# Optimization experiments

Hardware: AMD Instinct MI355X
Metric: run time of the kernel (lower is better)

Reference implementation:

```python
import jax, jax.numpy as jnp
import numpy as np

N_NODES = 50000
N_EDGES = 800000
N_FEAT = 128
N_HID = 256
N_PAIRS = 100000


def _gcn_norm(edge_index, n_nodes):
    # add self loops, compute D^-1/2 (A+I) D^-1/2 edge weights (PyG gcn_norm)
    loops = jnp.arange(n_nodes, dtype=edge_index.dtype)
    row = jnp.concatenate([edge_index[0], loops])
    col = jnp.concatenate([edge_index[1], loops])
    deg = jax.ops.segment_sum(jnp.ones_like(col, dtype=jnp.float32), col,
                              num_segments=n_nodes)
    dinv = jnp.where(deg > 0, jax.lax.rsqrt(deg), 0.0)
    norm = dinv[row] * dinv[col]  # [E + N]
    return row, col, norm


def _gcn_conv(x, W, b, row, col, norm, n_nodes):
    h = x @ W                       # [N, out]
    msg = h[row] * norm[:, None]    # gather + scale  [E+N, out]
    agg = jax.ops.segment_sum(msg, col, num_segments=n_nodes)  # scatter-add
    return agg + b


def setup_inputs() -> dict:
    key = jax.random.key(0)
    ks = jax.random.split(key, 9)
    edge_index = jax.random.randint(ks[0], (2, N_EDGES), 0, N_NODES, dtype=jnp.int64)
    features = jax.random.normal(ks[1], (N_NODES, N_FEAT), dtype=jnp.float32)
    mask = jax.random.randint(ks[2], (N_PAIRS, 2), 0, N_NODES, dtype=jnp.int64)
    s1 = 1.0 / np.sqrt(N_FEAT)
    s2 = 1.0 / np.sqrt(N_HID)
    W1 = jax.random.uniform(ks[3], (N_FEAT, N_HID), jnp.float32, -s1, s1)
    b1 = jnp.zeros((N_HID,), jnp.float32)
    W2 = jax.random.uniform(ks[4], (N_HID, N_FEAT), jnp.float32, -s2, s2)
    b2 = jnp.zeros((N_FEAT,), jnp.float32)
    Wl = jax.random.uniform(ks[5], (N_HID, 1), jnp.float32, -s2, s2)
    bl = jax.random.uniform(ks[6], (1,), jnp.float32, -s2, s2)
    return {"edge_index": edge_index, "features": features, "mask": mask,
            "W1": W1, "b1": b1, "W2": W2, "b2": b2, "Wl": Wl, "bl": bl}


def reference(edge_index, features, mask, W1, b1, W2, b2, Wl, bl):
    n = features.shape[0]
    row, col, norm = _gcn_norm(edge_index, n)
    h = _gcn_conv(features, W1, b1, row, col, norm, n)   # GCNConv a
    h = jax.nn.relu(h)                                   # dropout p=0 -> identity
    h = _gcn_conv(h, W2, b2, row, col, norm, n)          # GCNConv b
    mt = mask.T
    p1 = jax.lax.stop_gradient(h[mt[0]])                 # .detach()
    p2 = jax.lax.stop_gradient(h[mt[1]])
    hp = jnp.concatenate([p1, p2], axis=1)               # [n_pairs, 2*n_feat]
    return jax.nn.sigmoid(hp @ Wl + bl)
```

## Files before the change

### kernel.cpp

```cpp
#include <hip/hip_runtime.h>
#include <math.h>

#define NFEAT 128
#define NHID 256
#define NBLK 128

typedef __attribute__((ext_vector_type(8))) short short8;
typedef __attribute__((ext_vector_type(4))) float f32x4;
typedef __attribute__((ext_vector_type(2))) float f32x2;

__device__ inline unsigned short f2bf(float f) {
  unsigned u = __float_as_uint(f);
  u += 0x7fffu + ((u >> 16) & 1u);
  return (unsigned short)(u >> 16);
}
__device__ inline float bflo(unsigned u) { return __uint_as_float(u << 16); }
__device__ inline float bfhi(unsigned u) { return __uint_as_float(u & 0xffff0000u); }


__device__ inline void packOne(const float* __restrict__ W,
                               unsigned short* __restrict__ Wp, int idx, int KS,
                               int OUT) {
  int lane = idx & 63;
  int t = idx >> 6;
  int ks = t % KS;
  int nt = t / KS;
  int n = nt * 16 + (lane & 15);
  int k0 = ks * 32 + (lane >> 4) * 8;
  unsigned short v[8];
#pragma unroll
  for (int j = 0; j < 8; j++) v[j] = f2bf(W[(size_t)(k0 + j) * OUT + n]);
  *reinterpret_cast<short8*>(Wp + (size_t)idx * 8) =
      *reinterpret_cast<short8*>(v);
}

__global__ __launch_bounds__(1024) void k_hist_pack(
    const int* __restrict__ col, int* __restrict__ hist2d, int nE, int nb,
    const float* __restrict__ W1, const float* __restrict__ W2,
    unsigned short* __restrict__ W1p, unsigned short* __restrict__ W2p) {
  if (blockIdx.x >= NBLK) {
    int idx = (blockIdx.x - NBLK) * 1024 + threadIdx.x;
    if (idx < 4096) packOne(W1, W1p, idx, 4, 256);
    else packOne(W2, W2p, idx - 4096, 8, 128);
    return;
  }
  __shared__ int h[1024];
  for (int i = threadIdx.x; i < nb; i += 1024) h[i] = 0;
  __syncthreads();
  int chunk = (nE + NBLK - 1) / NBLK;
  int beg = blockIdx.x * chunk, end = min(beg + chunk, nE);
  for (int e = beg + threadIdx.x; e < end; e += 1024)
    atomicAdd(&h[col[e] >> 6], 1);
  __syncthreads();
  for (int i = threadIdx.x; i < nb; i += 1024)
    hist2d[i * NBLK + blockIdx.x] = h[i];
}

__global__ __launch_bounds__(256) void k_bsum(const int* __restrict__ a,
                                              int* __restrict__ psum, int S,
                                              const float* __restrict__ b2,
                                              const float* __restrict__ Wl,
                                              const float* __restrict__ bl,
                                              float* __restrict__ Cbuf) {
  int t = threadIdx.x;
  if (blockIdx.x == gridDim.x - 1) {
    float v = (t < 128) ? b2[t] * (Wl[t] + Wl[128 + t]) : 0.f;
#pragma unroll
    for (int o = 32; o; o >>= 1) v += __shfl_down(v, o);
    __shared__ float fw[4];
    if ((t & 63) == 0) fw[t >> 6] = v;
    __syncthreads();
    if (t == 0) Cbuf[0] = fw[0] + fw[1] + fw[2] + fw[3] + bl[0];
    return;
  }
  int i = blockIdx.x * 256 + t;
  int v = (i < S) ? a[i] : 0;
#pragma unroll
  for (int o = 32; o; o >>= 1) v += __shfl_down(v, o);
  __shared__ int ws[4];
  if ((t & 63) == 0) ws[t >> 6] = v;
  __syncthreads();
  if (t == 0) psum[blockIdx.x] = ws[0] + ws[1] + ws[2] + ws[3];
}

__global__ __launch_bounds__(256) void k_s3m(const int* __restrict__ a,
                                             const int* __restrict__ psum,
                                             int* __restrict__ out, int S) {
  __shared__ int sh[256];
  __shared__ int ws[4];
  int t = threadIdx.x;
  int b = blockIdx.x;
  int partial = 0;
  for (int i = t; i < b; i += 256) partial += psum[i];
#pragma unroll
  for (int o = 32; o; o >>= 1) partial += __shfl_down(partial, o);
  if ((t & 63) == 0) ws[t >> 6] = partial;
  int i = b * 256 + t;
  int d = (i < S) ? a[i] : 0;
  sh[t] = d;
  __syncthreads();
  int base = ws[0] + ws[1] + ws[2] + ws[3];
  for (int o = 1; o < 256; o <<= 1) {
    int u = (t >= o) ? sh[t - o] : 0;
    __syncthreads();
    sh[t] += u;
    __syncthreads();
  }
  if (i < S) out[i] = base + sh[t] - d;
}

__global__ __launch_bounds__(1024) void k_part2(const int* __restrict__ row,
                                                const int* __restrict__ col,
                                                const int* __restrict__ sbase,
                                                unsigned* __restrict__ tmp,
                                                int nE, int nb) {
  __shared__ int cur[1024];
  for (int i = threadIdx.x; i < nb; i += 1024)
    cur[i] = sbase[i * NBLK + blockIdx.x];
  __syncthreads();
  int chunk = (nE + NBLK - 1) / NBLK;
  int beg = blockIdx.x * chunk, end = min(beg + chunk, nE);
  for (int e = beg + threadIdx.x; e < end; e += 1024) {
    int c = col[e];
    int pos = atomicAdd(&cur[c >> 6], 1);
    tmp[pos] = ((unsigned)(c & 63) << 16) | (unsigned)row[e];
  }
}

__global__ __launch_bounds__(256) void k_bsort_cvt(
    const unsigned* __restrict__ tmp, const int* __restrict__ sbase,
    int* __restrict__ ebuf, int* __restrict__ offs, float* __restrict__ dinv,
    const float* __restrict__ feat, unsigned short* __restrict__ xs, int n,
    int nE, int nb) {
  __shared__ int bins[64], cur[64];
  __shared__ float sdinv[64];
  int b = blockIdx.x;
  int beg = sbase[b * NBLK];
  int end = (b == nb - 1) ? nE : sbase[(b + 1) * NBLK];
  int t = threadIdx.x;
  if (t == 0 && b == nb - 1) offs[n] = nE;
  if (t < 64) bins[t] = 0;
  __syncthreads();
  for (int i = beg + t; i < end; i += 256) atomicAdd(&bins[tmp[i] >> 16], 1);
  __syncthreads();
  if (t < 64) {
    int v = bins[t];
    int s = v;
#pragma unroll
    for (int o = 1; o < 64; o <<= 1) {
      int u = __shfl_up(s, o);
      if (t >= o) s += u;
    }
    int off = beg + s - v;
    cur[t] = off;
    float dv = rsqrtf((float)(v + 1));
    sdinv[t] = dv;
    int node = b * 64 + t;
    if (node < n) {
      offs[node] = off;
      dinv[node] = dv;
    }
  }
  __syncthreads();
  for (int i = beg + t; i < end; i += 256) {
    unsigned p = tmp[i];
    int pos = atomicAdd(&cur[p >> 16], 1);
    ebuf[pos] = (int)(p & 0xffffu);
  }
  for (int i = t; i < 64 * 32; i += 256) {
    int r = i >> 5;
    int node = b * 64 + r;
    if (node >= n) break;
    float d = sdinv[r];
    float4 v = reinterpret_cast<const float4*>(feat)[(size_t)node * 32 + (i & 31)];
    unsigned short o[4] = {f2bf(v.x * d), f2bf(v.y * d), f2bf(v.z * d),
                           f2bf(v.w * d)};
    reinterpret_cast<ushort4*>(xs)[(size_t)node * 32 + (i & 31)] =
        *reinterpret_cast<ushort4*>(o);
  }
}

__global__ __launch_bounds__(256) void k_fused(
    const char* __restrict__ Gb, const int* __restrict__ offs,
    const int* __restrict__ ebuf, const float* __restrict__ dinv,
    const unsigned short* __restrict__ B1p, const unsigned short* __restrict__ B2p,
    const float* __restrict__ b1, const float* __restrict__ Wl,
    float* __restrict__ P, int n) {
  __shared__ __align__(16) unsigned short sh_z[32 * 128];
  __shared__ __align__(16) unsigned short sh1[32 * 264];
  __shared__ float pacc[32][2];
  int rt0 = blockIdx.x * 2;
  int wave = threadIdx.x >> 6;
  int lane = threadIdx.x & 63;
  int quad = lane >> 4;
  if (threadIdx.x < 64) pacc[threadIdx.x >> 1][threadIdx.x & 1] = 0.f;

  {
    int g = lane >> 4;
    int c = lane & 15;
    unsigned cb = (unsigned)c << 4;
    int rbase = rt0 * 16;
    for (int it = 0; it < 8; ++it) {
      int rin = wave * 8 + it;
      int node = rbase + rin;
      f32x2 acc[4] = {};
      float d = 0.f;
      if (node < n) {
        d = dinv[node];
        int beg = offs[node], end = offs[node + 1];
        if (g == 0) {
          uint4 s = *reinterpret_cast<const uint4*>(
              Gb + (((unsigned)node << 8) | cb));
          acc[0] = (f32x2){bflo(s.x), bfhi(s.x)};
          acc[1] = (f32x2){bflo(s.y), bfhi(s.y)};
          acc[2] = (f32x2){bflo(s.z), bfhi(s.z)};
          acc[3] = (f32x2){bflo(s.w), bfhi(s.w)};
        }
        int e = beg + g;
        for (; e + 4 < end; e += 8) {
          int i0 = ebuf[e], i1 = ebuf[e + 4];
          uint4 v0 = *reinterpret_cast<const uint4*>(
              Gb + (((unsigned)i0 << 8) | cb));
          uint4 v1 = *reinterpret_cast<const uint4*>(
              Gb + (((unsigned)i1 << 8) | cb));
          acc[0] += (f32x2){bflo(v0.x), bfhi(v0.x)};
          acc[1] += (f32x2){bflo(v0.y), bfhi(v0.y)};
          acc[2] += (f32x2){bflo(v0.z), bfhi(v0.z)};
          acc[3] += (f32x2){bflo(v0.w), bfhi(v0.w)};
          acc[0] += (f32x2){bflo(v1.x), bfhi(v1.x)};
          acc[1] += (f32x2){bflo(v1.y), bfhi(v1.y)};
          acc[2] += (f32x2){bflo(v1.z), bfhi(v1.z)};
          acc[3] += (f32x2){bflo(v1.w), bfhi(v1.w)};
        }
        if (e < end) {
          uint4 v0 = *reinterpret_cast<const uint4*>(
              Gb + (((unsigned)ebuf[e] << 8) | cb));
          acc[0] += (f32x2){bflo(v0.x), bfhi(v0.x)};
          acc[1] += (f32x2){bflo(v0.y), bfhi(v0.y)};
          acc[2] += (f32x2){bflo(v0.z), bfhi(v0.z)};
          acc[3] += (f32x2){bflo(v0.w), bfhi(v0.w)};
        }
      }
#pragma unroll
      for (int j = 0; j < 4; j++) {
        acc[j].x += __shfl_down(acc[j].x, 32);
        acc[j].y += __shfl_down(acc[j].y, 32);
        acc[j].x += __shfl_down(acc[j].x, 16);
        acc[j].y += __shfl_down(acc[j].y, 16);
      }
      if (g == 0) {
        unsigned o[4];
#pragma unroll
        for (int k = 0; k < 4; k++)
          o[k] = (unsigned)f2bf(acc[k].x * d) |
                 ((unsigned)f2bf(acc[k].y * d) << 16);
        int c_swz = c ^ (rin & 7);
        *reinterpret_cast<uint4*>(sh_z + rin * 128 + c_swz * 8) =
            *reinterpret_cast<uint4*>(o);
      }
    }
  }
  __syncthreads();

  f32x4 acc[2][4] = {};
  int r0a = lane & 15;
  int xsw = lane & 7;
#pragma unroll
  for (int ks = 0; ks < 4; ks++) {
    int cA = quad + ks * 4;
    int cS = (cA ^ xsw) * 8;
    short8 a0 = *reinterpret_cast<const short8*>(sh_z + r0a * 128 + cS);
    short8 a1 = *reinterpret_cast<const short8*>(sh_z + (16 + r0a) * 128 + cS);
#pragma unroll
    for (int ct = 0; ct < 4; ct++) {
      int nt = wave * 4 + ct;
      short8 b = *reinterpret_cast<const short8*>(
          B1p + ((size_t)(nt * 4 + ks) * 64 + lane) * 8);
      acc[0][ct] = __builtin_amdgcn_mfma_f32_16x16x32_bf16(a0, b, acc[0][ct], 0, 0, 0);
      acc[1][ct] = __builtin_amdgcn_mfma_f32_16x16x32_bf16(a1, b, acc[1][ct], 0, 0, 0);
    }
  }
#pragma unroll
  for (int ct = 0; ct < 4; ct++) {
    int c = (wave * 4 + ct) * 16 + (lane & 15);
    float bv = b1[c];
#pragma unroll
    for (int rg = 0; rg < 2; rg++)
#pragma unroll
      for (int i = 0; i < 4; i++) {
        float v = fmaxf(acc[rg][ct][i] + bv, 0.f);
        sh1[(rg * 16 + quad * 4 + i) * 264 + c] = f2bf(v);
      }
  }
  __syncthreads();

  f32x4 acc2[2][2] = {};
  const unsigned short* a2_0 = sh1 + (size_t)(lane & 15) * 264 + quad * 8;
  const unsigned short* a2_1 = sh1 + (size_t)(16 + (lane & 15)) * 264 + quad * 8;
#pragma unroll
  for (int ks = 0; ks < 8; ks++) {
    short8 a0 = *reinterpret_cast<const short8*>(a2_0 + ks * 32);
    short8 a1 = *reinterpret_cast<const short8*>(a2_1 + ks * 32);
#pragma unroll
    for (int ct = 0; ct < 2; ct++) {
      int nt = wave * 2 + ct;
      short8 b = *reinterpret_cast<const short8*>(
          B2p + ((size_t)(nt * 8 + ks) * 64 + lane) * 8);
      acc2[0][ct] = __builtin_amdgcn_mfma_f32_16x16x32_bf16(a0, b, acc2[0][ct], 0, 0, 0);
      acc2[1][ct] = __builtin_amdgcn_mfma_f32_16x16x32_bf16(a1, b, acc2[1][ct], 0, 0, 0);
    }
  }
  float p1[2][4] = {}, p2[2][4] = {};
#pragma unroll
  for (int rg = 0; rg < 2; rg++) {
    int r0 = (rt0 + rg) * 16 + quad * 4;
    float dv[4];
#pragma unroll
    for (int i = 0; i < 4; i++) dv[i] = dinv[r0 + i];
#pragma unroll
    for (int ct = 0; ct < 2; ct++) {
      int c = (wave * 2 + ct) * 16 + (lane & 15);
      float wl1 = Wl[c], wl2 = Wl[128 + c];
#pragma unroll
      for (int i = 0; i < 4; i++) {
        float v = acc2[rg][ct][i] * dv[i];
        p1[rg][i] = fmaf(v, wl1, p1[rg][i]);
        p2[rg][i] = fmaf(v, wl2, p2[rg][i]);
      }
    }
  }
#pragma unroll
  for (int rg = 0; rg < 2; rg++)
#pragma unroll
    for (int i = 0; i < 4; i++) {
#pragma unroll
      for (int o = 8; o; o >>= 1) {
        p1[rg][i] += __shfl_xor(p1[rg][i], o);
        p2[rg][i] += __shfl_xor(p2[rg][i], o);
      }
    }
  if ((lane & 15) == 0) {
#pragma unroll
    for (int rg = 0; rg < 2; rg++)
#pragma unroll
      for (int i = 0; i < 4; i++) {
        int row = rg * 16 + quad * 4 + i;
        atomicAdd(&pacc[row][0], p1[rg][i]);
        atomicAdd(&pacc[row][1], p2[rg][i]);
      }
  }
  __syncthreads();
// ... 19 lines not shown
    sy += v.y;
  }
  sx += __shfl_down(sx, 2);
  sy += __shfl_down(sy, 2);
  sx += __shfl_down(sx, 1);
  sy += __shfl_down(sy, 1);
  if (sub == 0) {
    float2 self = p[i];
    float d = dinv[i];
    q[i] = make_float2((sx + self.x) * d, (sy + self.y) * d);
  }
}

__global__ __launch_bounds__(256) void k_head2(const float2* __restrict__ q,
                                               const int* __restrict__ mask,
                                               const float* __restrict__ Cbuf,
                                               float* __restrict__ out, int P) {
  int p = blockIdx.x * 256 + threadIdx.x;
  if (p >= P) return;
  int m0 = mask[2 * p], m1 = mask[2 * p + 1];
  float s = q[m0].x + q[m1].y + Cbuf[0];
  out[p] = 1.0f / (1.0f + expf(-s));
}

extern "C" void kernel_launch(void* const* d_in, const int* in_sizes, int n_in,
                              void* d_out, int out_size, void* d_ws,
                              size_t ws_size, hipStream_t stream) {
  const int* edge = (const int*)d_in[0];
  const float* feat = (const float*)d_in[1];
  const int* mask = (const int*)d_in[2];
  const float* W1 = (const float*)d_in[3];
  const float* b1 = (const float*)d_in[4];
  const float* W2 = (const float*)d_in[5];
  const float* b2 = (const float*)d_in[6];
  const float* Wl = (const float*)d_in[7];
  const float* bl = (const float*)d_in[8];
  float* out = (float*)d_out;

  const int E = in_sizes[0] / 2;
  const int N = in_sizes[1] / NFEAT;
  const int P = in_sizes[2] / 2;
  const int* rowp = edge;
  const int* colp = edge + E;
  const int nrt = N / 16;
  const int nb = (N + 63) / 64;
  const int S = nb * NBLK;
  const int nS = (S + 255) / 256;

  auto aln = [](size_t x) { return (x + 255) & ~(size_t)255; };
  char* w = (char*)d_ws;
  int* hist2d = (int*)w;           w += aln((size_t)S * 4);
  int* sbase = (int*)w;            w += aln((size_t)S * 4);
  int* psum = (int*)w;             w += aln((size_t)1024 * 4);
  float* Cbuf = (float*)w;         w += aln(256);
  int* offs = (int*)w;             w += aln((size_t)(N + 1) * 4);
  int* ebuf = (int*)w;             w += aln((size_t)E * 4);
  unsigned* tmp = (unsigned*)w;    w += aln((size_t)E * 4);
  float* dinv = (float*)w;         w += aln((size_t)N * 4 + 1024);
  unsigned short* xs = (unsigned short*)w;  w += aln((size_t)N * NFEAT * 2);
  float* p = (float*)w;            w += aln((size_t)(N + 32) * 8);
  float2* q = (float2*)w;          w += aln((size_t)N * 8);
  unsigned short* W1p = (unsigned short*)w; w += aln((size_t)NFEAT * NHID * 2);
  unsigned short* W2p = (unsigned short*)w; w += aln((size_t)NHID * NFEAT * 2);

  k_hist_pack<<<NBLK + 8, 1024, 0, stream>>>(colp, hist2d, E, nb, W1, W2, W1p,
                                             W2p);
  k_bsum<<<nS + 1, 256, 0, stream>>>(hist2d, psum, S, b2, Wl, bl, Cbuf);
  k_s3m<<<nS, 256, 0, stream>>>(hist2d, psum, sbase, S);
  k_part2<<<NBLK, 1024, 0, stream>>>(rowp, colp, sbase, tmp, E, nb);
  k_bsort_cvt<<<nb, 256, 0, stream>>>(tmp, sbase, ebuf, offs, dinv, feat, xs,
                                      N, E, nb);
  k_fused<<<(nrt + 1) / 2, 256, 0, stream>>>((const char*)xs, offs, ebuf, dinv,
                                             W1p, W2p, b1, Wl, p, N);
  k_agg_s<<<(N + 63) / 64, 256, 0, stream>>>((const float2*)p, offs, ebuf,
                                             dinv, q, N);
  k_head2<<<(P + 255) / 256, 256, 0, stream>>>(q, mask, Cbuf, out, P);
}
```

Baseline: 180.7 us.

## Interleave two-node gathers, privatize sort bins per wave, alias shared buffers

The fused aggregation loop now processes two destination nodes at once, issuing four independent row gathers per iteration to raise memory-level parallelism. The bucket-sort kernel gives each wave its own histogram and cursor copies, cutting LDS atomic contention, and the partition block count grows from 128 to 256. The fused kernel reuses one LDS buffer for both stages by loading the A fragments into registers behind an extra barrier, which reduces shared memory per block to allow more occupancy. The cost is higher register pressure and more code.

```diff
diff --git a/kernel.cpp b/kernel.cpp
--- a/kernel.cpp
+++ b/kernel.cpp
@@ -3,7 +3,7 @@
 
 #define NFEAT 128
 #define NHID 256
-#define NBLK 128
+#define NBLK 256
 
 typedef __attribute__((ext_vector_type(8))) short short8;
 typedef __attribute__((ext_vector_type(4))) float f32x4;
@@ -132,19 +132,22 @@
     int* __restrict__ ebuf, int* __restrict__ offs, float* __restrict__ dinv,
     const float* __restrict__ feat, unsigned short* __restrict__ xs, int n,
     int nE, int nb) {
-  __shared__ int bins[64], cur[64];
+  __shared__ int bins[4][64], cur4[4][64];
   __shared__ float sdinv[64];
   int b = blockIdx.x;
   int beg = sbase[b * NBLK];
   int end = (b == nb - 1) ? nE : sbase[(b + 1) * NBLK];
   int t = threadIdx.x;
+  int w4 = t >> 6;
   if (t == 0 && b == nb - 1) offs[n] = nE;
-  if (t < 64) bins[t] = 0;
-  __syncthreads();
-  for (int i = beg + t; i < end; i += 256) atomicAdd(&bins[tmp[i] >> 16], 1);
+  bins[w4][t & 63] = 0;
+  __syncthreads();
+  for (int i = beg + t; i < end; i += 256)
+    atomicAdd(&bins[w4][tmp[i] >> 16], 1);
   __syncthreads();
   if (t < 64) {
-    int v = bins[t];
+    int b0 = bins[0][t], b1 = bins[1][t], b2 = bins[2][t], b3 = bins[3][t];
+    int v = b0 + b1 + b2 + b3;
     int s = v;
 #pragma unroll
     for (int o = 1; o < 64; o <<= 1) {
@@ -152,7 +155,10 @@
       if (t >= o) s += u;
     }
     int off = beg + s - v;
-    cur[t] = off;
+    cur4[0][t] = off;
+    cur4[1][t] = off + b0;
+    cur4[2][t] = off + b0 + b1;
+    cur4[3][t] = off + b0 + b1 + b2;
     float dv = rsqrtf((float)(v + 1));
     sdinv[t] = dv;
     int node = b * 64 + t;
@@ -164,7 +170,7 @@
   __syncthreads();
   for (int i = beg + t; i < end; i += 256) {
     unsigned p = tmp[i];
-    int pos = atomicAdd(&cur[p >> 16], 1);
+    int pos = atomicAdd(&cur4[w4][p >> 16], 1);
     ebuf[pos] = (int)(p & 0xffffu);
   }
   for (int i = t; i < 64 * 32; i += 256) {
@@ -186,8 +192,7 @@
     const unsigned short* __restrict__ B1p, const unsigned short* __restrict__ B2p,
     const float* __restrict__ b1, const float* __restrict__ Wl,
     float* __restrict__ P, int n) {
-  __shared__ __align__(16) unsigned short sh_z[32 * 128];
-  __shared__ __align__(16) unsigned short sh1[32 * 264];
+  __shared__ __align__(16) unsigned short sh[32 * 264];
   __shared__ float pacc[32][2];
   int rt0 = blockIdx.x * 2;
   int wave = threadIdx.x >> 6;
@@ -197,87 +202,159 @@
 
   {
     int g = lane >> 4;
-    int c = lane & 15;
-    unsigned cb = (unsigned)c << 4;
+    int cidx = lane & 15;
+    unsigned cb = (unsigned)cidx << 4;
     int rbase = rt0 * 16;
-    for (int it = 0; it < 8; ++it) {
-      int rin = wave * 8 + it;
-      int node = rbase + rin;
-      f32x2 acc[4] = {};
-      float d = 0.f;
-      if (node < n) {
-        d = dinv[node];
-        int beg = offs[node], end = offs[node + 1];
+    for (int it = 0; it < 8; it += 2) {
+      int rinA = wave * 8 + it, rinB = rinA + 1;
+      int nodeA = rbase + rinA, nodeB = rbase + rinB;
+      f32x2 aA[4] = {}, aB[4] = {};
+      float dA = 0.f, dB = 0.f;
+      int eA = 0, endA = 0, eB = 0, endB = 0;
+      if (nodeA < n) {
+        dA = dinv[nodeA];
+        eA = offs[nodeA] + g;
+        endA = offs[nodeA + 1];
         if (g == 0) {
           uint4 s = *reinterpret_cast<const uint4*>(
-              Gb + (((unsigned)node << 8) | cb));
-          acc[0] = (f32x2){bflo(s.x), bfhi(s.x)};
-          acc[1] = (f32x2){bflo(s.y), bfhi(s.y)};
-          acc[2] = (f32x2){bflo(s.z), bfhi(s.z)};
-          acc[3] = (f32x2){bflo(s.w), bfhi(s.w)};
+              Gb + (((unsigned)nodeA << 8) | cb));
+          aA[0] = (f32x2){bflo(s.x), bfhi(s.x)};
+          aA[1] = (f32x2){bflo(s.y), bfhi(s.y)};
+          aA[2] = (f32x2){bflo(s.z), bfhi(s.z)};
+          aA[3] = (f32x2){bflo(s.w), bfhi(s.w)};
         }
-        int e = beg + g;
-        for (; e + 4 < end; e += 8) {
-          int i0 = ebuf[e], i1 = ebuf[e + 4];
-          uint4 v0 = *reinterpret_cast<const uint4*>(
-              Gb + (((unsigned)i0 << 8) | cb));
-          uint4 v1 = *reinterpret_cast<const uint4*>(
-              Gb + (((unsigned)i1 << 8) | cb));
-          acc[0] += (f32x2){bflo(v0.x), bfhi(v0.x)};
-          acc[1] += (f32x2){bflo(v0.y), bfhi(v0.y)};
-          acc[2] += (f32x2){bflo(v0.z), bfhi(v0.z)};
-          acc[3] += (f32x2){bflo(v0.w), bfhi(v0.w)};
-          acc[0] += (f32x2){bflo(v1.x), bfhi(v1.x)};
-          acc[1] += (f32x2){bflo(v1.y), bfhi(v1.y)};
-          acc[2] += (f32x2){bflo(v1.z), bfhi(v1.z)};
-          acc[3] += (f32x2){bflo(v1.w), bfhi(v1.w)};
+      }
+      if (nodeB < n) {
+        dB = dinv[nodeB];
+        eB = offs[nodeB] + g;
+        endB = offs[nodeB + 1];
+        if (g == 0) {
+          uint4 s = *reinterpret_cast<const uint4*>(
+              Gb + (((unsigned)nodeB << 8) | cb));
+          aB[0] = (f32x2){bflo(s.x), bfhi(s.x)};
+          aB[1] = (f32x2){bflo(s.y), bfhi(s.y)};
+          aB[2] = (f32x2){bflo(s.z), bfhi(s.z)};
+          aB[3] = (f32x2){bflo(s.w), bfhi(s.w)};
         }
-        if (e < end) {
-          uint4 v0 = *reinterpret_cast<const uint4*>(
-              Gb + (((unsigned)ebuf[e] << 8) | cb));
-          acc[0] += (f32x2){bflo(v0.x), bfhi(v0.x)};
-          acc[1] += (f32x2){bflo(v0.y), bfhi(v0.y)};
-          acc[2] += (f32x2){bflo(v0.z), bfhi(v0.z)};
-          acc[3] += (f32x2){bflo(v0.w), bfhi(v0.w)};
+      }
+      while (eA + 4 < endA && eB + 4 < endB) {
+        int i0 = ebuf[eA], i1 = ebuf[eA + 4];
+        int j0 = ebuf[eB], j1 = ebuf[eB + 4];
+        uint4 vA0 = *reinterpret_cast<const uint4*>(Gb + (((unsigned)i0 << 8) | cb));
+        uint4 vA1 = *reinterpret_cast<const uint4*>(Gb + (((unsigned)i1 << 8) | cb));
+        uint4 vB0 = *reinterpret_cast<const uint4*>(Gb + (((unsigned)j0 << 8) | cb));
+        uint4 vB1 = *reinterpret_cast<const uint4*>(Gb + (((unsigned)j1 << 8) | cb));
+        aA[0] += (f32x2){bflo(vA0.x), bfhi(vA0.x)};
+        aA[1] += (f32x2){bflo(vA0.y), bfhi(vA0.y)};
+        aA[2] += (f32x2){bflo(vA0.z), bfhi(vA0.z)};
+        aA[3] += (f32x2){bflo(vA0.w), bfhi(vA0.w)};
+        aA[0] += (f32x2){bflo(vA1.x), bfhi(vA1.x)};
+        aA[1] += (f32x2){bflo(vA1.y), bfhi(vA1.y)};
+        aA[2] += (f32x2){bflo(vA1.z), bfhi(vA1.z)};
+        aA[3] += (f32x2){bflo(vA1.w), bfhi(vA1.w)};
+        aB[0] += (f32x2){bflo(vB0.x), bfhi(vB0.x)};
+        aB[1] += (f32x2){bflo(vB0.y), bfhi(vB0.y)};
+        aB[2] += (f32x2){bflo(vB0.z), bfhi(vB0.z)};
+        aB[3] += (f32x2){bflo(vB0.w), bfhi(vB0.w)};
+        aB[0] += (f32x2){bflo(vB1.x), bfhi(vB1.x)};
+        aB[1] += (f32x2){bflo(vB1.y), bfhi(vB1.y)};
+        aB[2] += (f32x2){bflo(vB1.z), bfhi(vB1.z)};
+        aB[3] += (f32x2){bflo(vB1.w), bfhi(vB1.w)};
+        eA += 8;
+        eB += 8;
+      }
+      for (; eA + 4 < endA; eA += 8) {
+        int i0 = ebuf[eA], i1 = ebuf[eA + 4];
+        uint4 v0 = *reinterpret_cast<const uint4*>(Gb + (((unsigned)i0 << 8) | cb));
+        uint4 v1 = *reinterpret_cast<const uint4*>(Gb + (((unsigned)i1 << 8) | cb));
+        aA[0] += (f32x2){bflo(v0.x), bfhi(v0.x)};
+        aA[1] += (f32x2){bflo(v0.y), bfhi(v0.y)};
+        aA[2] += (f32x2){bflo(v0.z), bfhi(v0.z)};
+        aA[3] += (f32x2){bflo(v0.w), bfhi(v0.w)};
+        aA[0] += (f32x2){bflo(v1.x), bfhi(v1.x)};
+        aA[1] += (f32x2){bflo(v1.y), bfhi(v1.y)};
+        aA[2] += (f32x2){bflo(v1.z), bfhi(v1.z)};
+        aA[3] += (f32x2){bflo(v1.w), bfhi(v1.w)};
+      }
+      if (eA < endA) {
+        uint4 v0 = *reinterpret_cast<const uint4*>(
+            Gb + (((unsigned)ebuf[eA] << 8) | cb));
+        aA[0] += (f32x2){bflo(v0.x), bfhi(v0.x)};
+        aA[1] += (f32x2){bflo(v0.y), bfhi(v0.y)};
+        aA[2] += (f32x2){bflo(v0.z), bfhi(v0.z)};
+        aA[3] += (f32x2){bflo(v0.w), bfhi(v0.w)};
+      }
+      for (; eB + 4 < endB; eB += 8) {
+        int i0 = ebuf[eB], i1 = ebuf[eB + 4];
+        uint4 v0 = *reinterpret_cast<const uint4*>(Gb + (((unsigned)i0 << 8) | cb));
+        uint4 v1 = *reinterpret_cast<const uint4*>(Gb + (((unsigned)i1 << 8) | cb));
+        aB[0] += (f32x2){bflo(v0.x), bfhi(v0.x)};
+        aB[1] += (f32x2){bflo(v0.y), bfhi(v0.y)};
+        aB[2] += (f32x2){bflo(v0.z), bfhi(v0.z)};
+        aB[3] += (f32x2){bflo(v0.w), bfhi(v0.w)};
+        aB[0] += (f32x2){bflo(v1.x), bfhi(v1.x)};
+        aB[1] += (f32x2){bflo(v1.y), bfhi(v1.y)};
+        aB[2] += (f32x2){bflo(v1.z), bfhi(v1.z)};
+        aB[3] += (f32x2){bflo(v1.w), bfhi(v1.w)};
+      }
+      if (eB < endB) {
+        uint4 v0 = *reinterpret_cast<const uint4*>(
+            Gb + (((unsigned)ebuf[eB] << 8) | cb));
+        aB[0] += (f32x2){bflo(v0.x), bfhi(v0.x)};
+        aB[1] += (f32x2){bflo(v0.y), bfhi(v0.y)};
+        aB[2] += (f32x2){bflo(v0.z), bfhi(v0.z)};
+        aB[3] += (f32x2){bflo(v0.w), bfhi(v0.w)};
+      }
+#pragma unroll
+      for (int j = 0; j < 4; j++) {
+        aA[j].x += __shfl_down(aA[j].x, 32);
+        aA[j].y += __shfl_down(aA[j].y, 32);
+        aB[j].x += __shfl_down(aB[j].x, 32);
+        aB[j].y += __shfl_down(aB[j].y, 32);
+        aA[j].x += __shfl_down(aA[j].x, 16);
+        aA[j].y += __shfl_down(aA[j].y, 16);
+        aB[j].x += __shfl_down(aB[j].x, 16);
+        aB[j].y += __shfl_down(aB[j].y, 16);
+      }
+      if (g == 0) {
+        unsigned oA[4], oB[4];
+#pragma unroll
+        for (int k = 0; k < 4; k++) {
+          oA[k] = (unsigned)f2bf(aA[k].x * dA) |
+                  ((unsigned)f2bf(aA[k].y * dA) << 16);
+          oB[k] = (unsigned)f2bf(aB[k].x * dB) |
+                  ((unsigned)f2bf(aB[k].y * dB) << 16);
         }
-      }
-#pragma unroll
-      for (int j = 0; j < 4; j++) {
-        acc[j].x += __shfl_down(acc[j].x, 32);
-        acc[j].y += __shfl_down(acc[j].y, 32);
-        acc[j].x += __shfl_down(acc[j].x, 16);
-        acc[j].y += __shfl_down(acc[j].y, 16);
-      }
-      if (g == 0) {
-        unsigned o[4];
-#pragma unroll
-        for (int k = 0; k < 4; k++)
-          o[k] = (unsigned)f2bf(acc[k].x * d) |
-                 ((unsigned)f2bf(acc[k].y * d) << 16);
-        int c_swz = c ^ (rin & 7);
-        *reinterpret_cast<uint4*>(sh_z + rin * 128 + c_swz * 8) =
-            *reinterpret_cast<uint4*>(o);
-      }
-    }
-  }
-  __syncthreads();
-
-  f32x4 acc[2][4] = {};
+        *reinterpret_cast<uint4*>(sh + rinA * 128 + (cidx ^ (rinA & 7)) * 8) =
+            *reinterpret_cast<uint4*>(oA);
+        *reinterpret_cast<uint4*>(sh + rinB * 128 + (cidx ^ (rinB & 7)) * 8) =
+            *reinterpret_cast<uint4*>(oB);
+      }
+    }
+  }
+  __syncthreads();
+
   int r0a = lane & 15;
   int xsw = lane & 7;
+  short8 fa0[4], fa1[4];
 #pragma unroll
   for (int ks = 0; ks < 4; ks++) {
-    int cA = quad + ks * 4;
-    int cS = (cA ^ xsw) * 8;
-    short8 a0 = *reinterpret_cast<const short8*>(sh_z + r0a * 128 + cS);
-    short8 a1 = *reinterpret_cast<const short8*>(sh_z + (16 + r0a) * 128 + cS);
+    int cS = ((quad + ks * 4) ^ xsw) * 8;
+    fa0[ks] = *reinterpret_cast<const short8*>(sh + r0a * 128 + cS);
+    fa1[ks] = *reinterpret_cast<const short8*>(sh + (16 + r0a) * 128 + cS);
+  }
+  __syncthreads();
+
+  f32x4 acc[2][4] = {};
+#pragma unroll
+  for (int ks = 0; ks < 4; ks++) {
 #pragma unroll
     for (int ct = 0; ct < 4; ct++) {
       int nt = wave * 4 + ct;
       short8 b = *reinterpret_cast<const short8*>(
           B1p + ((size_t)(nt * 4 + ks) * 64 + lane) * 8);
-      acc[0][ct] = __builtin_amdgcn_mfma_f32_16x16x32_bf16(a0, b, acc[0][ct], 0, 0, 0);
-      acc[1][ct] = __builtin_amdgcn_mfma_f32_16x16x32_bf16(a1, b, acc[1][ct], 0, 0, 0);
+      acc[0][ct] = __builtin_amdgcn_mfma_f32_16x16x32_bf16(fa0[ks], b, acc[0][ct], 0, 0, 0);
+      acc[1][ct] = __builtin_amdgcn_mfma_f32_16x16x32_bf16(fa1[ks], b, acc[1][ct], 0, 0, 0);
     }
   }
 #pragma unroll
@@ -289,14 +366,14 @@
 #pragma unroll
       for (int i = 0; i < 4; i++) {
         float v = fmaxf(acc[rg][ct][i] + bv, 0.f);
-        sh1[(rg * 16 + quad * 4 + i) * 264 + c] = f2bf(v);
+        sh[(rg * 16 + quad * 4 + i) * 264 + c] = f2bf(v);
       }
   }
   __syncthreads();
 
   f32x4 acc2[2][2] = {};
-  const unsigned short* a2_0 = sh1 + (size_t)(lane & 15) * 264 + quad * 8;
-  const unsigned short* a2_1 = sh1 + (size_t)(16 + (lane & 15)) * 264 + quad * 8;
+  const unsigned short* a2_0 = sh + (size_t)(lane & 15) * 264 + quad * 8;
+  const unsigned short* a2_1 = sh + (size_t)(16 + (lane & 15)) * 264 + quad * 8;
 #pragma unroll
   for (int ks = 0; ks < 8; ks++) {
     short8 a0 = *reinterpret_cast<const short8*>(a2_0 + ks * 32);
```

New measurement: 179.5 us. Within noise of the previous version (-0.7%).

## Merge CSR build stages into one cooperative kernel with grid syncs

Applied to the files above, without the earlier changes.

Replaces the five preprocessing launches (histogram plus weight packing, two-level prefix scan, partition, bucket sort plus feature conversion) with a single cooperative kernel that separates phases with grid.sync, doubling the number of partition blocks. The aim is to remove launch gaps and small-kernel overhead. Sort bins are also split per wave to cut LDS atomic contention. The gather loop in k_fused now loads 64 edge indices per wave and broadcasts them with shuffles, keeping four row loads in flight, and the two LDS buffers are merged to lower shared-memory use. The trade-off is that grid-wide barriers need all 256 blocks of 1024 threads to be co-resident, with a fallback to the old launches if the cooperative launch fails.

```diff
diff --git a/kernel.cpp b/kernel.cpp
--- a/kernel.cpp
+++ b/kernel.cpp
@@ -1,9 +1,12 @@
 #include <hip/hip_runtime.h>
+#include <hip/hip_cooperative_groups.h>
 #include <math.h>
+
+namespace cg = cooperative_groups;
 
 #define NFEAT 128
 #define NHID 256
-#define NBLK 128
+#define NBLK 256
 
 typedef __attribute__((ext_vector_type(8))) short short8;
 typedef __attribute__((ext_vector_type(4))) float f32x4;
@@ -16,7 +19,6 @@
 }
 __device__ inline float bflo(unsigned u) { return __uint_as_float(u << 16); }
 __device__ inline float bfhi(unsigned u) { return __uint_as_float(u & 0xffff0000u); }
-
 
 __device__ inline void packOne(const float* __restrict__ W,
                                unsigned short* __restrict__ Wp, int idx, int KS,
@@ -34,6 +36,151 @@
       *reinterpret_cast<short8*>(v);
 }
 
+__global__ __launch_bounds__(1024) void k_build(
+    const int* __restrict__ col, const int* __restrict__ row,
+    int* __restrict__ hist2d, int* __restrict__ sbase, int* __restrict__ T,
+    int* __restrict__ B, unsigned* __restrict__ tmp, int* __restrict__ ebuf,
+    int* __restrict__ offs, float* __restrict__ dinv,
+    const float* __restrict__ feat, unsigned short* __restrict__ xs,
+    const float* __restrict__ W1, const float* __restrict__ W2,
+    unsigned short* __restrict__ W1p, unsigned short* __restrict__ W2p,
+    const float* __restrict__ b2, const float* __restrict__ Wl,
+    const float* __restrict__ bl, float* __restrict__ Cbuf, int nE, int n,
+    int nb) {
+  cg::grid_group grid = cg::this_grid();
+  __shared__ int smi[2048];
+  __shared__ float sdinv[64];
+  int t = threadIdx.x;
+  int b = blockIdx.x;
+  int chunk = (nE + NBLK - 1) / NBLK;
+  int ebeg = b * chunk, eend = min(ebeg + chunk, nE);
+
+  for (int i = t; i < nb; i += 1024) smi[i] = 0;
+  __syncthreads();
+  for (int e = ebeg + t; e < eend; e += 1024) atomicAdd(&smi[col[e] >> 6], 1);
+  if (b < 8) {
+    int idx = b * 1024 + t;
+    if (idx < 4096) packOne(W1, W1p, idx, 4, 256);
+    else packOne(W2, W2p, idx - 4096, 8, 128);
+  }
+  if (b == 255) {
+    float v = (t < 128) ? b2[t] * (Wl[t] + Wl[128 + t]) : 0.f;
+#pragma unroll
+    for (int o = 32; o; o >>= 1) v += __shfl_down(v, o);
+    if (t == 0) sdinv[0] = v;
+    if (t == 64) sdinv[1] = v;
+    __syncthreads();
+    if (t == 0) Cbuf[0] = sdinv[0] + sdinv[1] + bl[0];
+  }
+  __syncthreads();
+  for (int i = t; i < nb; i += 1024) hist2d[i * NBLK + b] = smi[i];
+  __threadfence();
+  grid.sync();
+
+  {
+    int sub = t >> 8, tc = t & 255;
+    int bkt = b * 4 + sub;
+    int v = (bkt < nb) ? hist2d[bkt * NBLK + tc] : 0;
+    smi[sub * 256 + tc] = v;
+    __syncthreads();
+    for (int o = 1; o < 256; o <<= 1) {
+      int u = (tc >= o) ? smi[sub * 256 + tc - o] : 0;
+      __syncthreads();
+      smi[sub * 256 + tc] += u;
+      __syncthreads();
+    }
+    if (bkt < nb) {
+      sbase[bkt * NBLK + tc] = smi[sub * 256 + tc] - v;
+      if (tc == 255) T[bkt] = smi[sub * 256 + 255];
+    }
+  }
+  __threadfence();
+  grid.sync();
+
+  if (b == 0) {
+    int v = (t < nb) ? T[t] : 0;
+    smi[t] = v;
+    __syncthreads();
+    for (int o = 1; o < 1024; o <<= 1) {
+      int u = (t >= o) ? smi[t - o] : 0;
+      __syncthreads();
+      smi[t] += u;
+      __syncthreads();
+    }
+    if (t < nb) B[t] = smi[t] - v;
+    __threadfence();
+  }
+  grid.sync();
+
+  for (int i = t; i < nb; i += 1024) smi[i] = sbase[i * NBLK + b] + B[i];
+  __syncthreads();
+  for (int e = ebeg + t; e < eend; e += 1024) {
+    int c = col[e];
+    int pos = atomicAdd(&smi[c >> 6], 1);
+    tmp[pos] = ((unsigned)(c & 63) << 16) | (unsigned)row[e];
+  }
+  __threadfence();
+  grid.sync();
+
+  if (b == 0 && t == 0) offs[n] = nE;
+  int w16 = t >> 6;
+  for (int bk = b; bk < nb; bk += NBLK) {
+    int sbeg = B[bk] + sbase[bk * NBLK];
+    int send = (bk == nb - 1) ? nE : (B[bk + 1] + sbase[(bk + 1) * NBLK]);
+    smi[t] = 0;
+    smi[1024 + t] = 0;
+    __syncthreads();
+    for (int i = sbeg + t; i < send; i += 1024)
+      atomicAdd(&smi[w16 * 64 + (tmp[i] >> 16)], 1);
+    __syncthreads();
+    if (t < 64) {
+      int tot = 0;
+#pragma unroll
+      for (int j = 0; j < 16; j++) tot += smi[j * 64 + t];
+      int s = tot;
+#pragma unroll
+      for (int o = 1; o < 64; o <<= 1) {
+        int u = __shfl_up(s, o);
+        if (t >= o) s += u;
+      }
+      int off = sbeg + s - tot;
+      int run = off;
+#pragma unroll
+      for (int j = 0; j < 16; j++) {
+        smi[1024 + j * 64 + t] = run;
+        run += smi[j * 64 + t];
+      }
+      float dv = rsqrtf((float)(tot + 1));
+      sdinv[t] = dv;
+      int node = bk * 64 + t;
+      if (node < n) {
+        offs[node] = off;
+        dinv[node] = dv;
+      }
+    }
+    __syncthreads();
+    for (int i = sbeg + t; i < send; i += 1024) {
+      unsigned p = tmp[i];
+      int pos = atomicAdd(&smi[1024 + w16 * 64 + (p >> 16)], 1);
+      ebuf[pos] = (int)(p & 0xffffu);
+    }
+    for (int i = t; i < 2048; i += 1024) {
+      int r = i >> 5;
+      int node = bk * 64 + r;
+      if (node < n) {
+        float d = sdinv[r];
+        float4 v =
+            reinterpret_cast<const float4*>(feat)[(size_t)node * 32 + (i & 31)];
+        unsigned short o[4] = {f2bf(v.x * d), f2bf(v.y * d), f2bf(v.z * d),
+                               f2bf(v.w * d)};
+        reinterpret_cast<ushort4*>(xs)[(size_t)node * 32 + (i & 31)] =
+            *reinterpret_cast<ushort4*>(o);
+      }
+    }
+    __syncthreads();
+  }
+}
+
 __global__ __launch_bounds__(1024) void k_hist_pack(
     const int* __restrict__ col, int* __restrict__ hist2d, int nE, int nb,
     const float* __restrict__ W1, const float* __restrict__ W2,
@@ -132,19 +279,22 @@
     int* __restrict__ ebuf, int* __restrict__ offs, float* __restrict__ dinv,
     const float* __restrict__ feat, unsigned short* __restrict__ xs, int n,
     int nE, int nb) {
-  __shared__ int bins[64], cur[64];
+  __shared__ int bins[4][64], cur4[4][64];
   __shared__ float sdinv[64];
   int b = blockIdx.x;
   int beg = sbase[b * NBLK];
   int end = (b == nb - 1) ? nE : sbase[(b + 1) * NBLK];
   int t = threadIdx.x;
+  int w4 = t >> 6;
   if (t == 0 && b == nb - 1) offs[n] = nE;
-  if (t < 64) bins[t] = 0;
-  __syncthreads();
-  for (int i = beg + t; i < end; i += 256) atomicAdd(&bins[tmp[i] >> 16], 1);
+  bins[w4][t & 63] = 0;
+  __syncthreads();
+  for (int i = beg + t; i < end; i += 256)
+    atomicAdd(&bins[w4][tmp[i] >> 16], 1);
   __syncthreads();
   if (t < 64) {
-    int v = bins[t];
+    int b0 = bins[0][t], b1 = bins[1][t], b2 = bins[2][t], b3 = bins[3][t];
+    int v = b0 + b1 + b2 + b3;
     int s = v;
 #pragma unroll
     for (int o = 1; o < 64; o <<= 1) {
@@ -152,7 +302,10 @@
       if (t >= o) s += u;
     }
     int off = beg + s - v;
-    cur[t] = off;
+    cur4[0][t] = off;
+    cur4[1][t] = off + b0;
+    cur4[2][t] = off + b0 + b1;
+    cur4[3][t] = off + b0 + b1 + b2;
     float dv = rsqrtf((float)(v + 1));
     sdinv[t] = dv;
     int node = b * 64 + t;
@@ -164,7 +317,7 @@
   __syncthreads();
   for (int i = beg + t; i < end; i += 256) {
     unsigned p = tmp[i];
-    int pos = atomicAdd(&cur[p >> 16], 1);
+    int pos = atomicAdd(&cur4[w4][p >> 16], 1);
     ebuf[pos] = (int)(p & 0xffffu);
   }
   for (int i = t; i < 64 * 32; i += 256) {
@@ -180,14 +333,19 @@
   }
 }
 
+#define ACC2(A, V)                        \
+  A[0] += (f32x2){bflo(V.x), bfhi(V.x)};  \
+  A[1] += (f32x2){bflo(V.y), bfhi(V.y)};  \
+  A[2] += (f32x2){bflo(V.z), bfhi(V.z)};  \
+  A[3] += (f32x2){bflo(V.w), bfhi(V.w)};
+
 __global__ __launch_bounds__(256) void k_fused(
     const char* __restrict__ Gb, const int* __restrict__ offs,
     const int* __restrict__ ebuf, const float* __restrict__ dinv,
     const unsigned short* __restrict__ B1p, const unsigned short* __restrict__ B2p,
     const float* __restrict__ b1, const float* __restrict__ Wl,
     float* __restrict__ P, int n) {
-  __shared__ __align__(16) unsigned short sh_z[32 * 128];
-  __shared__ __align__(16) unsigned short sh1[32 * 264];
+  __shared__ __align__(16) unsigned short sh[32 * 264];
   __shared__ float pacc[32][2];
   int rt0 = blockIdx.x * 2;
   int wave = threadIdx.x >> 6;
@@ -197,8 +355,8 @@
 
   {
     int g = lane >> 4;
-    int c = lane & 15;
-    unsigned cb = (unsigned)c << 4;
+    int cidx = lane & 15;
+    unsigned cb = (unsigned)cidx << 4;
     int rbase = rt0 * 16;
     for (int it = 0; it < 8; ++it) {
       int rin = wave * 8 + it;
@@ -208,37 +366,46 @@
       if (node < n) {
         d = dinv[node];
         int beg = offs[node], end = offs[node + 1];
+        int deg = end - beg;
         if (g == 0) {
           uint4 s = *reinterpret_cast<const uint4*>(
               Gb + (((unsigned)node << 8) | cb));
-          acc[0] = (f32x2){bflo(s.x), bfhi(s.x)};
-          acc[1] = (f32x2){bflo(s.y), bfhi(s.y)};
-          acc[2] = (f32x2){bflo(s.z), bfhi(s.z)};
-          acc[3] = (f32x2){bflo(s.w), bfhi(s.w)};
+          ACC2(acc, s);
         }
-        int e = beg + g;
-        for (; e + 4 < end; e += 8) {
-          int i0 = ebuf[e], i1 = ebuf[e + 4];
-          uint4 v0 = *reinterpret_cast<const uint4*>(
-              Gb + (((unsigned)i0 << 8) | cb));
-          uint4 v1 = *reinterpret_cast<const uint4*>(
-              Gb + (((unsigned)i1 << 8) | cb));
-          acc[0] += (f32x2){bflo(v0.x), bfhi(v0.x)};
-          acc[1] += (f32x2){bflo(v0.y), bfhi(v0.y)};
-          acc[2] += (f32x2){bflo(v0.z), bfhi(v0.z)};
-          acc[3] += (f32x2){bflo(v0.w), bfhi(v0.w)};
-          acc[0] += (f32x2){bflo(v1.x), bfhi(v1.x)};
-          acc[1] += (f32x2){bflo(v1.y), bfhi(v1.y)};
-          acc[2] += (f32x2){bflo(v1.z), bfhi(v1.z)};
-          acc[3] += (f32x2){bflo(v1.w), bfhi(v1.w)};
-        }
-        if (e < end) {
-          uint4 v0 = *reinterpret_cast<const uint4*>(
-              Gb + (((unsigned)ebuf[e] << 8) | cb));
-          acc[0] += (f32x2){bflo(v0.x), bfhi(v0.x)};
-          acc[1] += (f32x2){bflo(v0.y), bfhi(v0.y)};
-          acc[2] += (f32x2){bflo(v0.z), bfhi(v0.z)};
-          acc[3] += (f32x2){bflo(v0.w), bfhi(v0.w)};
+        int kb = 0;
+        while (kb < deg) {
+          int m = min(deg - kb, 64);
+          int myi = beg + kb + lane;
+          int idx = (myi < end) ? ebuf[myi] : 0;
+          int j = 0;
+          for (; j + 16 <= m; j += 16) {
+            int s0 = __shfl(idx, j + g);
+            int s1 = __shfl(idx, j + 4 + g);
+            int s2 = __shfl(idx, j + 8 + g);
+            int s3 = __shfl(idx, j + 12 + g);
+            uint4 v0 = *reinterpret_cast<const uint4*>(Gb + (((unsigned)s0 << 8) | cb));
+            uint4 v1 = *reinterpret_cast<const uint4*>(Gb + (((unsigned)s1 << 8) | cb));
+            uint4 v2 = *reinterpret_cast<const uint4*>(Gb + (((unsigned)s2 << 8) | cb));
+            uint4 v3 = *reinterpret_cast<const uint4*>(Gb + (((unsigned)s3 << 8) | cb));
+            ACC2(acc, v0);
+            ACC2(acc, v1);
+            ACC2(acc, v2);
+            ACC2(acc, v3);
+          }
+          for (; j + 4 <= m; j += 4) {
+            int s0 = __shfl(idx, j + g);
+            uint4 v0 = *reinterpret_cast<const uint4*>(Gb + (((unsigned)s0 << 8) | cb));
+            ACC2(acc, v0);
+          }
+          int r = m - j;
+          if (r > 0) {
+            int s0 = __shfl(idx, j + ((g < r) ? g : 0));
+            if (g < r) {
+              uint4 v0 = *reinterpret_cast<const uint4*>(Gb + (((unsigned)s0 << 8) | cb));
+              ACC2(acc, v0);
+            }
+          }
+          kb += 64;
         }
       }
 #pragma unroll
@@ -254,30 +421,34 @@
         for (int k = 0; k < 4; k++)
           o[k] = (unsigned)f2bf(acc[k].x * d) |
                  ((unsigned)f2bf(acc[k].y * d) << 16);
-        int c_swz = c ^ (rin & 7);
-        *reinterpret_cast<uint4*>(sh_z + rin * 128 + c_swz * 8) =
+        *reinterpret_cast<uint4*>(sh + rin * 128 + (cidx ^ (rin & 7)) * 8) =
             *reinterpret_cast<uint4*>(o);
       }
     }
   }
   __syncthreads();
 
-  f32x4 acc[2][4] = {};
   int r0a = lane & 15;
   int xsw = lane & 7;
+  short8 fa0[4], fa1[4];
 #pragma unroll
   for (int ks = 0; ks < 4; ks++) {
-    int cA = quad + ks * 4;
-    int cS = (cA ^ xsw) * 8;
-    short8 a0 = *reinterpret_cast<const short8*>(sh_z + r0a * 128 + cS);
-    short8 a1 = *reinterpret_cast<const short8*>(sh_z + (16 + r0a) * 128 + cS);
+    int cS = ((quad + ks * 4) ^ xsw) * 8;
+    fa0[ks] = *reinterpret_cast<const short8*>(sh + r0a * 128 + cS);
+    fa1[ks] = *reinterpret_cast<const short8*>(sh + (16 + r0a) * 128 + cS);
+  }
+  __syncthreads();
+
+  f32x4 acc[2][4] = {};
+#pragma unroll
+  for (int ks = 0; ks < 4; ks++) {
 #pragma unroll
     for (int ct = 0; ct < 4; ct++) {
       int nt = wave * 4 + ct;
       short8 b = *reinterpret_cast<const short8*>(
           B1p + ((size_t)(nt * 4 + ks) * 64 + lane) * 8);
-      acc[0][ct] = __builtin_amdgcn_mfma_f32_16x16x32_bf16(a0, b, acc[0][ct], 0, 0, 0);
-      acc[1][ct] = __builtin_amdgcn_mfma_f32_16x16x32_bf16(a1, b, acc[1][ct], 0, 0, 0);
+      acc[0][ct] = __builtin_amdgcn_mfma_f32_16x16x32_bf16(fa0[ks], b, acc[0][ct], 0, 0, 0);
+      acc[1][ct] = __builtin_amdgcn_mfma_f32_16x16x32_bf16(fa1[ks], b, acc[1][ct], 0, 0, 0);
     }
   }
 #pragma unroll
@@ -289,14 +460,14 @@
 #pragma unroll
       for (int i = 0; i < 4; i++) {
         float v = fmaxf(acc[rg][ct][i] + bv, 0.f);
-        sh1[(rg * 16 + quad * 4 + i) * 264 + c] = f2bf(v);
+        sh[(rg * 16 + quad * 4 + i) * 264 + c] = f2bf(v);
       }
   }
   __syncthreads();
 
   f32x4 acc2[2][2] = {};
-  const unsigned short* a2_0 = sh1 + (size_t)(lane & 15) * 264 + quad * 8;
-  const unsigned short* a2_1 = sh1 + (size_t)(16 + (lane & 15)) * 264 + quad * 8;
+  const unsigned short* a2_0 = sh + (size_t)(lane & 15) * 264 + quad * 8;
+  const unsigned short* a2_1 = sh + (size_t)(16 + (lane & 15)) * 264 + quad * 8;
 #pragma unroll
   for (int ks = 0; ks < 8; ks++) {
     short8 a0 = *reinterpret_cast<const short8*>(a2_0 + ks * 32);
@@ -422,6 +593,7 @@
   int* hist2d = (int*)w;           w += aln((size_t)S * 4);
   int* sbase = (int*)w;            w += aln((size_t)S * 4);
   int* psum = (int*)w;             w += aln((size_t)1024 * 4);
+  int* Bq = (int*)w;               w += aln((size_t)1024 * 4);
   float* Cbuf = (float*)w;         w += aln(256);
   int* offs = (int*)w;             w += aln((size_t)(N + 1) * 4);
   int* ebuf = (int*)w;             w += aln((size_t)E * 4);
@@ -433,13 +605,28 @@
   unsigned short* W1p = (unsigned short*)w; w += aln((size_t)NFEAT * NHID * 2);
   unsigned short* W2p = (unsigned short*)w; w += aln((size_t)NHID * NFEAT * 2);
 
-  k_hist_pack<<<NBLK + 8, 1024, 0, stream>>>(colp, hist2d, E, nb, W1, W2, W1p,
-                                             W2p);
-  k_bsum<<<nS + 1, 256, 0, stream>>>(hist2d, psum, S, b2, Wl, bl, Cbuf);
-  k_s3m<<<nS, 256, 0, stream>>>(hist2d, psum, sbase, S);
-  k_part2<<<NBLK, 1024, 0, stream>>>(rowp, colp, sbase, tmp, E, nb);
-  k_bsort_cvt<<<nb, 256, 0, stream>>>(tmp, sbase, ebuf, offs, dinv, feat, xs,
-                                      N, E, nb);
+  {
+    int nE_ = E, n_ = N, nb_ = nb;
+    void* kb[] = {(void*)&colp, (void*)&rowp, (void*)&hist2d, (void*)&sbase,
+                  (void*)&psum, (void*)&Bq,   (void*)&tmp,    (void*)&ebuf,
+                  (void*)&offs, (void*)&dinv, (void*)&feat,   (void*)&xs,
+                  (void*)&W1,   (void*)&W2,   (void*)&W1p,    (void*)&W2p,
+                  (void*)&b2,   (void*)&Wl,   (void*)&bl,     (void*)&Cbuf,
+                  (void*)&nE_,  (void*)&n_,   (void*)&nb_};
+    hipError_t ce = hipLaunchCooperativeKernel((const void*)k_build,
+                                               dim3(NBLK), dim3(1024), kb, 0,
+                                               stream);
+    if (ce != hipSuccess) {
+      (void)hipGetLastError();
+      k_hist_pack<<<NBLK + 8, 1024, 0, stream>>>(colp, hist2d, E, nb, W1, W2,
+                                                 W1p, W2p);
+      k_bsum<<<nS + 1, 256, 0, stream>>>(hist2d, psum, S, b2, Wl, bl, Cbuf);
+      k_s3m<<<nS, 256, 0, stream>>>(hist2d, psum, sbase, S);
+      k_part2<<<NBLK, 1024, 0, stream>>>(rowp, colp, sbase, tmp, E, nb);
+      k_bsort_cvt<<<nb, 256, 0, stream>>>(tmp, sbase, ebuf, offs, dinv, feat,
+                                          xs, N, E, nb);
+    }
+  }
   k_fused<<<(nrt + 1) / 2, 256, 0, stream>>>((const char*)xs, offs, ebuf, dinv,
                                              W1p, W2p, b1, Wl, p, N);
   k_agg_s<<<(N + 63) / 64, 256, 0, stream>>>((const float2*)p, offs, ebuf,
```

New measurement: 608.7 us. 237% more time.

## Batch neighbor index loads via shuffles, reuse shared buffer, per-wave sort bins

Applied to the files above, without the earlier changes.

The gather loop now loads up to 64 neighbor indices per wave in a single coalesced read and hands them out with shuffles. It unrolls four row gathers per step to raise memory-level parallelism and cut dependent index loads. The two shared buffers are merged into one, with an extra barrier after the A fragments are loaded into registers, which lowers LDS use and may raise occupancy. The bucket sort keeps per-wave histograms and cursors to reduce shared atomic contention, and NBLK doubles to 256 for the scatter phase, which adds a barrier and some register pressure.

```diff
diff --git a/kernel.cpp b/kernel.cpp
--- a/kernel.cpp
+++ b/kernel.cpp
@@ -3,7 +3,7 @@
 
 #define NFEAT 128
 #define NHID 256
-#define NBLK 128
+#define NBLK 256
 
 typedef __attribute__((ext_vector_type(8))) short short8;
 typedef __attribute__((ext_vector_type(4))) float f32x4;
@@ -132,19 +132,22 @@
     int* __restrict__ ebuf, int* __restrict__ offs, float* __restrict__ dinv,
     const float* __restrict__ feat, unsigned short* __restrict__ xs, int n,
     int nE, int nb) {
-  __shared__ int bins[64], cur[64];
+  __shared__ int bins[4][64], cur4[4][64];
   __shared__ float sdinv[64];
   int b = blockIdx.x;
   int beg = sbase[b * NBLK];
   int end = (b == nb - 1) ? nE : sbase[(b + 1) * NBLK];
   int t = threadIdx.x;
+  int w4 = t >> 6;
   if (t == 0 && b == nb - 1) offs[n] = nE;
-  if (t < 64) bins[t] = 0;
-  __syncthreads();
-  for (int i = beg + t; i < end; i += 256) atomicAdd(&bins[tmp[i] >> 16], 1);
+  bins[w4][t & 63] = 0;
+  __syncthreads();
+  for (int i = beg + t; i < end; i += 256)
+    atomicAdd(&bins[w4][tmp[i] >> 16], 1);
   __syncthreads();
   if (t < 64) {
-    int v = bins[t];
+    int b0 = bins[0][t], b1 = bins[1][t], b2 = bins[2][t], b3 = bins[3][t];
+    int v = b0 + b1 + b2 + b3;
     int s = v;
 #pragma unroll
     for (int o = 1; o < 64; o <<= 1) {
@@ -152,7 +155,10 @@
       if (t >= o) s += u;
     }
     int off = beg + s - v;
-    cur[t] = off;
+    cur4[0][t] = off;
+    cur4[1][t] = off + b0;
+    cur4[2][t] = off + b0 + b1;
+    cur4[3][t] = off + b0 + b1 + b2;
     float dv = rsqrtf((float)(v + 1));
     sdinv[t] = dv;
     int node = b * 64 + t;
@@ -164,7 +170,7 @@
   __syncthreads();
   for (int i = beg + t; i < end; i += 256) {
     unsigned p = tmp[i];
-    int pos = atomicAdd(&cur[p >> 16], 1);
+    int pos = atomicAdd(&cur4[w4][p >> 16], 1);
     ebuf[pos] = (int)(p & 0xffffu);
   }
   for (int i = t; i < 64 * 32; i += 256) {
@@ -180,14 +186,19 @@
   }
 }
 
+#define ACC2(A, V)                        \
+  A[0] += (f32x2){bflo(V.x), bfhi(V.x)};  \
+  A[1] += (f32x2){bflo(V.y), bfhi(V.y)};  \
+  A[2] += (f32x2){bflo(V.z), bfhi(V.z)};  \
+  A[3] += (f32x2){bflo(V.w), bfhi(V.w)};
+
 __global__ __launch_bounds__(256) void k_fused(
     const char* __restrict__ Gb, const int* __restrict__ offs,
     const int* __restrict__ ebuf, const float* __restrict__ dinv,
     const unsigned short* __restrict__ B1p, const unsigned short* __restrict__ B2p,
     const float* __restrict__ b1, const float* __restrict__ Wl,
     float* __restrict__ P, int n) {
-  __shared__ __align__(16) unsigned short sh_z[32 * 128];
-  __shared__ __align__(16) unsigned short sh1[32 * 264];
+  __shared__ __align__(16) unsigned short sh[32 * 264];
   __shared__ float pacc[32][2];
   int rt0 = blockIdx.x * 2;
   int wave = threadIdx.x >> 6;
@@ -197,8 +208,8 @@
 
   {
     int g = lane >> 4;
-    int c = lane & 15;
-    unsigned cb = (unsigned)c << 4;
+    int cidx = lane & 15;
+    unsigned cb = (unsigned)cidx << 4;
     int rbase = rt0 * 16;
     for (int it = 0; it < 8; ++it) {
       int rin = wave * 8 + it;
@@ -208,37 +219,46 @@
       if (node < n) {
         d = dinv[node];
         int beg = offs[node], end = offs[node + 1];
+        int deg = end - beg;
         if (g == 0) {
           uint4 s = *reinterpret_cast<const uint4*>(
               Gb + (((unsigned)node << 8) | cb));
-          acc[0] = (f32x2){bflo(s.x), bfhi(s.x)};
-          acc[1] = (f32x2){bflo(s.y), bfhi(s.y)};
-          acc[2] = (f32x2){bflo(s.z), bfhi(s.z)};
-          acc[3] = (f32x2){bflo(s.w), bfhi(s.w)};
+          ACC2(acc, s);
         }
-        int e = beg + g;
-        for (; e + 4 < end; e += 8) {
-          int i0 = ebuf[e], i1 = ebuf[e + 4];
-          uint4 v0 = *reinterpret_cast<const uint4*>(
-              Gb + (((unsigned)i0 << 8) | cb));
-          uint4 v1 = *reinterpret_cast<const uint4*>(
-              Gb + (((unsigned)i1 << 8) | cb));
-          acc[0] += (f32x2){bflo(v0.x), bfhi(v0.x)};
-          acc[1] += (f32x2){bflo(v0.y), bfhi(v0.y)};
-          acc[2] += (f32x2){bflo(v0.z), bfhi(v0.z)};
-          acc[3] += (f32x2){bflo(v0.w), bfhi(v0.w)};
-          acc[0] += (f32x2){bflo(v1.x), bfhi(v1.x)};
-          acc[1] += (f32x2){bflo(v1.y), bfhi(v1.y)};
-          acc[2] += (f32x2){bflo(v1.z), bfhi(v1.z)};
-          acc[3] += (f32x2){bflo(v1.w), bfhi(v1.w)};
-        }
-        if (e < end) {
-          uint4 v0 = *reinterpret_cast<const uint4*>(
-              Gb + (((unsigned)ebuf[e] << 8) | cb));
-          acc[0] += (f32x2){bflo(v0.x), bfhi(v0.x)};
-          acc[1] += (f32x2){bflo(v0.y), bfhi(v0.y)};
-          acc[2] += (f32x2){bflo(v0.z), bfhi(v0.z)};
-          acc[3] += (f32x2){bflo(v0.w), bfhi(v0.w)};
+        int kb = 0;
+        while (kb < deg) {
+          int m = min(deg - kb, 64);
+          int myi = beg + kb + lane;
+          int idx = (myi < end) ? ebuf[myi] : 0;
+          int j = 0;
+          for (; j + 16 <= m; j += 16) {
+            int s0 = __shfl(idx, j + g);
+            int s1 = __shfl(idx, j + 4 + g);
+            int s2 = __shfl(idx, j + 8 + g);
+            int s3 = __shfl(idx, j + 12 + g);
+            uint4 v0 = *reinterpret_cast<const uint4*>(Gb + (((unsigned)s0 << 8) | cb));
+            uint4 v1 = *reinterpret_cast<const uint4*>(Gb + (((unsigned)s1 << 8) | cb));
+            uint4 v2 = *reinterpret_cast<const uint4*>(Gb + (((unsigned)s2 << 8) | cb));
+            uint4 v3 = *reinterpret_cast<const uint4*>(Gb + (((unsigned)s3 << 8) | cb));
+            ACC2(acc, v0);
+            ACC2(acc, v1);
+            ACC2(acc, v2);
+            ACC2(acc, v3);
+          }
+          for (; j + 4 <= m; j += 4) {
+            int s0 = __shfl(idx, j + g);
+            uint4 v0 = *reinterpret_cast<const uint4*>(Gb + (((unsigned)s0 << 8) | cb));
+            ACC2(acc, v0);
+          }
+          int r = m - j;
+          if (r > 0) {
+            int s0 = __shfl(idx, j + ((g < r) ? g : 0));
+            if (g < r) {
+              uint4 v0 = *reinterpret_cast<const uint4*>(Gb + (((unsigned)s0 << 8) | cb));
+              ACC2(acc, v0);
+            }
+          }
+          kb += 64;
         }
       }
 #pragma unroll
@@ -254,30 +274,34 @@
         for (int k = 0; k < 4; k++)
           o[k] = (unsigned)f2bf(acc[k].x * d) |
                  ((unsigned)f2bf(acc[k].y * d) << 16);
-        int c_swz = c ^ (rin & 7);
-        *reinterpret_cast<uint4*>(sh_z + rin * 128 + c_swz * 8) =
+        *reinterpret_cast<uint4*>(sh + rin * 128 + (cidx ^ (rin & 7)) * 8) =
             *reinterpret_cast<uint4*>(o);
       }
     }
   }
   __syncthreads();
 
-  f32x4 acc[2][4] = {};
   int r0a = lane & 15;
   int xsw = lane & 7;
+  short8 fa0[4], fa1[4];
 #pragma unroll
   for (int ks = 0; ks < 4; ks++) {
-    int cA = quad + ks * 4;
-    int cS = (cA ^ xsw) * 8;
-    short8 a0 = *reinterpret_cast<const short8*>(sh_z + r0a * 128 + cS);
-    short8 a1 = *reinterpret_cast<const short8*>(sh_z + (16 + r0a) * 128 + cS);
+    int cS = ((quad + ks * 4) ^ xsw) * 8;
+    fa0[ks] = *reinterpret_cast<const short8*>(sh + r0a * 128 + cS);
+    fa1[ks] = *reinterpret_cast<const short8*>(sh + (16 + r0a) * 128 + cS);
+  }
+  __syncthreads();
+
+  f32x4 acc[2][4] = {};
+#pragma unroll
+  for (int ks = 0; ks < 4; ks++) {
 #pragma unroll
     for (int ct = 0; ct < 4; ct++) {
       int nt = wave * 4 + ct;
       short8 b = *reinterpret_cast<const short8*>(
           B1p + ((size_t)(nt * 4 + ks) * 64 + lane) * 8);
-      acc[0][ct] = __builtin_amdgcn_mfma_f32_16x16x32_bf16(a0, b, acc[0][ct], 0, 0, 0);
-      acc[1][ct] = __builtin_amdgcn_mfma_f32_16x16x32_bf16(a1, b, acc[1][ct], 0, 0, 0);
+      acc[0][ct] = __builtin_amdgcn_mfma_f32_16x16x32_bf16(fa0[ks], b, acc[0][ct], 0, 0, 0);
+      acc[1][ct] = __builtin_amdgcn_mfma_f32_16x16x32_bf16(fa1[ks], b, acc[1][ct], 0, 0, 0);
     }
   }
 #pragma unroll
@@ -289,14 +313,14 @@
 #pragma unroll
       for (int i = 0; i < 4; i++) {
         float v = fmaxf(acc[rg][ct][i] + bv, 0.f);
-        sh1[(rg * 16 + quad * 4 + i) * 264 + c] = f2bf(v);
+        sh[(rg * 16 + quad * 4 + i) * 264 + c] = f2bf(v);
       }
   }
   __syncthreads();
 
   f32x4 acc2[2][2] = {};
-  const unsigned short* a2_0 = sh1 + (size_t)(lane & 15) * 264 + quad * 8;
-  const unsigned short* a2_1 = sh1 + (size_t)(16 + (lane & 15)) * 264 + quad * 8;
+  const unsigned short* a2_0 = sh + (size_t)(lane & 15) * 264 + quad * 8;
+  const unsigned short* a2_1 = sh + (size_t)(16 + (lane & 15)) * 264 + quad * 8;
 #pragma unroll
   for (int ks = 0; ks < 8; ks++) {
     short8 a0 = *reinterpret_cast<const short8*>(a2_0 + ks * 32);
```

After: 179.0 us. About the same (-1.0%).
